# Optimization experiments

Hardware: AMD Instinct MI355X
Metric: run time of the kernel (lower is better)

## Reference

```python
import jax, jax.numpy as jnp
import numpy as np

B, S, D, H = 2, 2048, 1024, 16
DK = D // H


def setup_inputs() -> dict:
    key = jax.random.key(0)
    ks = jax.random.split(key, 7)
    q = jax.random.normal(ks[0], (B, S, D), dtype=jnp.float32)
    k = jax.random.normal(ks[1], (B, S, D), dtype=jnp.float32)
    v = jax.random.normal(ks[2], (B, S, D), dtype=jnp.float32)
    # causal mask, broadcastable [B,1,S,S]; masked_fill where mask==0
    mask = jnp.broadcast_to(jnp.tril(jnp.ones((S, S), dtype=jnp.int32)), (B, 1, S, S))
    scale = 0.02
    Wq = jax.random.normal(ks[3], (D, D), dtype=jnp.float32) * scale
    Wk = jax.random.normal(ks[4], (D, D), dtype=jnp.float32) * scale
    Wv = jax.random.normal(ks[5], (D, D), dtype=jnp.float32) * scale
    Wo = jax.random.normal(ks[6], (D, D), dtype=jnp.float32) * scale
    return {"q": q, "k": k, "v": v, "mask": mask, "Wq": Wq, "Wk": Wk, "Wv": Wv, "Wo": Wo}


def reference(q, k, v, mask, Wq, Wk, Wv, Wo):
    # torch nn.Linear(bias=False): y = x @ W.T with W of shape [out, in]
    def proj(x, W):
        return (x @ W.T).reshape(B, S, H, DK).transpose(0, 2, 1, 3)  # [B,H,S,DK]

    Q = proj(q, Wq)
    K = proj(k, Wk)
    V = proj(v, Wv)
    inv_sqrt_dk = np.float32(1.0 / np.sqrt(DK))
    scores = jnp.einsum('bhqd,bhkd->bhqk', Q, K) * inv_sqrt_dk  # [B,H,S,S]
    scores = jnp.where(mask == 0, jnp.float32(-jnp.inf), scores)
    attn = jax.nn.softmax(scores, axis=-1)
    x = jnp.einsum('bhqk,bhkd->bhqd', attn, V)  # [B,H,S,DK]
    x = x.transpose(0, 2, 1, 3).reshape(B, S, D)
    return x @ Wo.T
```

## Files before the change

kernel.cpp:

```cpp
#include <hip/hip_runtime.h>

typedef __bf16 bf16x8 __attribute__((ext_vector_type(8)));
typedef __bf16 bf16x2 __attribute__((ext_vector_type(2)));
typedef float  f32x4  __attribute__((ext_vector_type(4)));

#define DEV static __device__ __forceinline__
#define VMCNT(n) asm volatile("s_waitcnt vmcnt(" #n ")" ::: "memory")
#define LGKM0()  asm volatile("s_waitcnt lgkmcnt(0)" ::: "memory")
#define SBAR()   __builtin_amdgcn_s_barrier()
#define SFENCE() __builtin_amdgcn_sched_barrier(0)


DEV ushort f2bf(float f) {
    return __builtin_bit_cast(ushort, (__bf16)f);
}
DEV uint pk2(float a, float b) {
    bf16x2 t; t[0] = (__bf16)a; t[1] = (__bf16)b;
    return __builtin_bit_cast(uint, t);
}

DEV float redmax4(float x) {
    x = fmaxf(x, __shfl_xor(x, 16));
    return fmaxf(x, __shfl_xor(x, 32));
}
DEV float redsum4(float x) {
    x += __shfl_xor(x, 16);
    return x + __shfl_xor(x, 32);
}

DEV void stage_swz(const ushort* g, int gstride, char* lds, int nchunks) {
    const int tid  = threadIdx.x;
    const int lane = tid & 63;
    const int wave = tid >> 6;
    for (int c0 = wave * 64; c0 < nchunks; c0 += 256) {
        int c   = c0 + lane;
        int row = c >> 3;
        int cc  = (c & 7) ^ (row & 7);
        const ushort* src = g + row * gstride + cc * 8;
        __builtin_amdgcn_global_load_lds((__attribute__((address_space(1))) void*)src,
                                         (__attribute__((address_space(3))) void*)(lds + c0 * 16),
                                         16, 0, 0);
    }
}

DEV bf16x8 ldfrag(const char* tile, int row, int kc) {
    int off = (row << 7) + ((kc ^ (row & 7)) << 4);
    return *(const bf16x8*)(tile + off);
}


struct CvtArgs { const float* s[7]; ushort* d[7]; int n[7]; };

__global__ void cvt_kernel(CvtArgs a) {
    const int y = blockIdx.y;
    const float* __restrict__ s = a.s[y];
    ushort* __restrict__ d = a.d[y];
    const int n = a.n[y];
    const int stride = gridDim.x * blockDim.x;
    for (int i = blockIdx.x * blockDim.x + threadIdx.x; i * 8 < n; i += stride) {
        const float4* p = (const float4*)(s + (size_t)i * 8);
        float4 x = p[0], yv = p[1];
        uint4 o;
        o.x = pk2(x.x,  x.y);
        o.y = pk2(x.z,  x.w);
        o.z = pk2(yv.x, yv.y);
        o.w = pk2(yv.z, yv.w);
        *(uint4*)(d + (size_t)i * 8) = o;
    }
}


constexpr int GN = 1024, GK = 1024;

template<typename EPI>
DEV void gemm_body(const ushort* __restrict__ A, const ushort* __restrict__ W,
                   char* smem, EPI epi) {
    const int tid  = threadIdx.x;
    const int lane = tid & 63;
    const int w    = tid >> 6;
    const int wr   = w >> 1, wc = w & 1;
    const int hi   = lane >> 4, lj = lane & 15;
    const int nb   = blockIdx.x & 7, mb = blockIdx.x >> 3;

    f32x4 acc[4][4];
#pragma unroll
    for (int mi = 0; mi < 4; mi++)
#pragma unroll
        for (int ni = 0; ni < 4; ni++) acc[mi][ni] = f32x4{0.f, 0.f, 0.f, 0.f};

    const ushort* Ag = A + (size_t)mb * 128 * GK;
    const ushort* Wg = W + (size_t)nb * 128 * GK;

    for (int k0 = 0; k0 < GK; k0 += 64) {
        __syncthreads();
        stage_swz(Ag + k0, GK, smem, 1024);
        stage_swz(Wg + k0, GK, smem + 16384, 1024);
        __syncthreads();
#pragma unroll
        for (int kk = 0; kk < 2; ++kk) {
            bf16x8 a[4], b[4];
#pragma unroll
            for (int mi = 0; mi < 4; mi++) a[mi] = ldfrag(smem, wr * 64 + mi * 16 + lj, kk * 4 + hi);
#pragma unroll
            for (int ni = 0; ni < 4; ni++) b[ni] = ldfrag(smem + 16384, wc * 64 + ni * 16 + lj, kk * 4 + hi);
#pragma unroll
            for (int mi = 0; mi < 4; mi++)
#pragma unroll
                for (int ni = 0; ni < 4; ni++)
                    acc[mi][ni] = __builtin_amdgcn_mfma_f32_16x16x32_bf16(a[mi], b[ni], acc[mi][ni], 0, 0, 0);
        }
    }

#pragma unroll
    for (int mi = 0; mi < 4; mi++)
#pragma unroll
        for (int r = 0; r < 4; r++) {
            const int gm = mb * 128 + wr * 64 + mi * 16 + hi * 4 + r;
#pragma unroll
            for (int ni = 0; ni < 4; ni++) {
                const int gn = nb * 128 + wc * 64 + ni * 16 + lj;
                epi(gm, gn, acc[mi][ni][r]);
            }
        }
}

struct ProjArgs {
    const ushort* A[3]; const ushort* W[3]; ushort* O[3];
    float scale[3]; int mode[3];
};

__global__ __launch_bounds__(256, 3) void gemm_proj(ProjArgs args) {
    __shared__ char smem[32768];
    const int z = blockIdx.z;
    const ushort* A = args.A[z];
    const ushort* W = args.W[z];
    ushort* Out = args.O[z];
    const float scale = args.scale[z];
    const int mode = args.mode[z];
    gemm_body(A, W, smem, [&](int gm, int gn, float v) {
        v *= scale;
        const int b_ = gm >> 11, s_ = gm & 2047;
        const int h_ = gn >> 6,  d_ = gn & 63;
        size_t off;
        if (mode == 0) off = (((size_t)b_ * 16 + h_) * 2048 + s_) * 64 + d_;
        else           off = (((size_t)b_ * 16 + h_) * 64 + d_) * 2048 + s_;
        Out[off] = f2bf(v);
    });
}

__global__ __launch_bounds__(256, 3) void gemm_out(const ushort* __restrict__ A,
                                                   const ushort* __restrict__ W,
                                                   float* __restrict__ Out) {
    __shared__ char smem[32768];
    gemm_body(A, W, smem, [&](int gm, int gn, float v) {
        Out[(size_t)gm * GN + gn] = v;
    });
}


__global__ __launch_bounds__(256, 3) void attn_kernel(const ushort* __restrict__ Qb,
                                                      const ushort* __restrict__ Kb,
                                                      const ushort* __restrict__ Vt,
                                                      ushort* __restrict__ Xb,
                                                      float* __restrict__ Opart,
                                                      float* __restrict__ Mlp) {
    constexpr int S = 2048;
    __shared__ char smem[49152];
    const int tid = threadIdx.x, lane = tid & 63, w = tid >> 6;
    const int hi = lane >> 4, lj = lane & 15;
    char* Pw = smem + 32768 + w * 4096;
    const int bh = blockIdx.x;
    const int y = blockIdx.y;

    int qt, kts, kte, half;
    bool partial;
    if (y < 16) {
        qt = 15 - (y >> 1); half = y & 1; partial = true;
        if (half == 0) { kts = 0; kte = qt + 1; }
        else           { kts = qt + 1; kte = 2 * qt + 2; }
    } else {
        qt = 23 - y; half = 0; partial = false;
        kts = 0; kte = 2 * qt + 2;
    }
    const int q0 = qt * 128;
    const int q0w = q0 + w * 32;

    const ushort* Qg = Qb + (size_t)bh * S * 64;
    const ushort* Kg = Kb + (size_t)bh * S * 64;
    const ushort* Vg = Vt + (size_t)bh * 64 * S;

    bf16x8 qf[2][2];
#pragma unroll
    for (int mi = 0; mi < 2; mi++)
#pragma unroll
        for (int kk = 0; kk < 2; kk++)
            qf[mi][kk] = *(const bf16x8*)(Qg + (size_t)(q0w + mi * 16 + lj) * 64 + kk * 32 + hi * 8);

    f32x4 o[2][4];
    float m_run[2] = { -1e30f, -1e30f }, l_run[2] = { 0.f, 0.f };
#pragma unroll
    for (int mi = 0; mi < 2; mi++)
#pragma unroll
        for (int nd = 0; nd < 4; nd++) o[mi][nd] = f32x4{0.f, 0.f, 0.f, 0.f};

    stage_swz(Kg + (size_t)kts * 64 * 64, 64, smem, 512);
    stage_swz(Vg + kts * 64, S, smem + 16384, 512);
    int cur = 0;

    for (int t = kts; t < kte; ++t) {
        char* Kc = smem + (cur << 13);
        char* Vc = smem + 16384 + (cur << 13);
        if (t + 1 < kte) {
            stage_swz(Kg + (size_t)(t + 1) * 64 * 64, 64, smem + ((cur ^ 1) << 13), 512);
            stage_swz(Vg + (t + 1) * 64, S, smem + 16384 + ((cur ^ 1) << 13), 512);
            VMCNT(4);
        } else {
            VMCNT(0);
        }
        SBAR(); SFENCE();

        if (t * 64 <= q0w + 31) {
            f32x4 sc[2][4];
#pragma unroll
            for (int mi = 0; mi < 2; mi++)
#pragma unroll
                for (int ni = 0; ni < 4; ni++) sc[mi][ni] = f32x4{0.f, 0.f, 0.f, 0.f};
            __builtin_amdgcn_s_setprio(1);
#pragma unroll
            for (int kk = 0; kk < 2; ++kk) {
                bf16x8 kf[4];
#pragma unroll
                for (int ni = 0; ni < 4; ni++) kf[ni] = ldfrag(Kc, ni * 16 + lj, kk * 4 + hi);
#pragma unroll
                for (int mi = 0; mi < 2; mi++)
#pragma unroll
                    for (int ni = 0; ni < 4; ni++)
                        sc[mi][ni] = __builtin_amdgcn_mfma_f32_16x16x32_bf16(kf[ni], qf[mi][kk], sc[mi][ni], 0, 0, 0);
            }
            __builtin_amdgcn_s_setprio(0);

            const bool diag = (t * 64 + 63 > q0w);
#pragma unroll
            for (int mi = 0; mi < 2; mi++) {
                const int q = q0w + mi * 16 + lj;
                if (diag) {
#pragma unroll
                    for (int ni = 0; ni < 4; ni++)
#pragma unroll
                        for (int r = 0; r < 4; r++)
                            if (t * 64 + ni * 16 + hi * 4 + r > q) sc[mi][ni][r] = -1e30f;
                }
                float mx = -1e30f;
#pragma unroll
                for (int ni = 0; ni < 4; ni++)
#pragma unroll
                    for (int r = 0; r < 4; r++) mx = fmaxf(mx, sc[mi][ni][r]);
                mx = redmax4(mx);
                const float mo = m_run[mi];
                const bool defer = __all(mx <= mo + 8.f);
                float mn, rs;
                if (defer) { mn = mo; rs = 1.f; }
                else { mn = fmaxf(mo, mx); rs = __builtin_exp2f(mo - mn); m_run[mi] = mn; }
                float ps = 0.f;
                const int row = mi * 16 + lj;
#pragma unroll
                for (int ni = 0; ni < 4; ni++) {
                    float p0 = __builtin_exp2f(sc[mi][ni][0] - mn);
                    float p1 = __builtin_exp2f(sc[mi][ni][1] - mn);
                    float p2 = __builtin_exp2f(sc[mi][ni][2] - mn);
                    float p3 = __builtin_exp2f(sc[mi][ni][3] - mn);
                    ps += (p0 + p1) + (p2 + p3);
                    uint2 pv; pv.x = pk2(p0, p1); pv.y = pk2(p2, p3);
                    const int c = ni * 2 + (hi >> 1);
                    *(uint2*)(Pw + row * 128 + ((c ^ (row & 7)) << 4) + ((hi & 1) << 3)) = pv;
                }
                ps = redsum4(ps);
                if (defer) {
                    l_run[mi] += ps;
                } else {
                    l_run[mi] = l_run[mi] * rs + ps;
#pragma unroll
                    for (int r = 0; r < 4; r++) {
                        float rr = __shfl(rs, (lane & 48) | (hi * 4 + r));
#pragma unroll
                        for (int nd = 0; nd < 4; nd++) o[mi][nd][r] *= rr;
                    }
                }
            }

            LGKM0(); SFENCE();

            __builtin_amdgcn_s_setprio(1);
#pragma unroll
            for (int kk = 0; kk < 2; ++kk) {
                bf16x8 pa[2], bv[4];
#pragma unroll
                for (int mi = 0; mi < 2; mi++) pa[mi] = ldfrag(Pw, mi * 16 + lj, kk * 4 + hi);
#pragma unroll
                for (int nd = 0; nd < 4; nd++) bv[nd] = ldfrag(Vc, nd * 16 + lj, kk * 4 + hi);
#pragma unroll
                for (int mi = 0; mi < 2; mi++)
#pragma unroll
                    for (int nd = 0; nd < 4; nd++)
                        o[mi][nd] = __builtin_amdgcn_mfma_f32_16x16x32_bf16(pa[mi], bv[nd], o[mi][nd], 0, 0, 0);
            }
            __builtin_amdgcn_s_setprio(0);
        }

        LGKM0();
        SBAR(); SFENCE();
        cur ^= 1;
    }

    if (partial) {
        const int pidx = (((bh << 3) + (qt - 8)) << 1) + half;
        float* Op = Opart + (size_t)pidx * 8192;
        float* Ml = Mlp   + (size_t)pidx * 256;
#pragma unroll
        for (int mi = 0; mi < 2; mi++)
#pragma unroll
            for (int r = 0; r < 4; r++) {
                const int row = w * 32 + mi * 16 + hi * 4 + r;
#pragma unroll
                for (int nd = 0; nd < 4; nd++)
                    Op[row * 64 + nd * 16 + lj] = o[mi][nd][r];
            }
        if (hi == 0) {
#pragma unroll
            for (int mi = 0; mi < 2; mi++) {
                const int row = w * 32 + mi * 16 + lj;
                Ml[row * 2 + 0] = m_run[mi];
                Ml[row * 2 + 1] = l_run[mi];
            }
        }
    } else {
        const int b_ = bh >> 4, h_ = bh & 15;
#pragma unroll
        for (int mi = 0; mi < 2; mi++)
#pragma unroll
            for (int r = 0; r < 4; r++) {
                float lv = __shfl(l_run[mi], (lane & 48) | (hi * 4 + r));
                float inv = 1.f / lv;
                const int srow = q0w + mi * 16 + hi * 4 + r;
#pragma unroll
                for (int nd = 0; nd < 4; nd++)
                    Xb[((size_t)b_ * S + srow) * 1024 + h_ * 64 + nd * 16 + lj] =
                        f2bf(o[mi][nd][r] * inv);
            }
    }
}


__global__ __launch_bounds__(256) void attn_merge(const float* __restrict__ Op,
                                                  const float* __restrict__ Ml,
                                                  ushort* __restrict__ Xb) {
    const int bh = blockIdx.x;
    const int qt = 8 + blockIdx.y;
    const int tid = threadIdx.x;
    const int row = tid >> 1;
    const int c0 = (tid & 1) * 32;
    const int sbase = (((bh << 3) + (qt - 8)) << 1);
    const float* o0 = Op + (size_t)(sbase + 0) * 8192 + row * 64 + c0;
    const float* o1 = Op + (size_t)(sbase + 1) * 8192 + row * 64 + c0;
    const float* ml0 = Ml + (size_t)(sbase + 0) * 256 + row * 2;
    const float* ml1 = Ml + (size_t)(sbase + 1) * 256 + row * 2;
    const float m0 = ml0[0], l0 = ml0[1];
    const float m1 = ml1[0], l1 = ml1[1];
    const float m = fmaxf(m0, m1);
    const float a0 = __builtin_exp2f(m0 - m), a1 = __builtin_exp2f(m1 - m);
    const float inv = 1.f / (l0 * a0 + l1 * a1);
    const int b_ = bh >> 4, h_ = bh & 15;
    ushort* dst = Xb + ((size_t)b_ * 2048 + qt * 128 + row) * 1024 + h_ * 64 + c0;
#pragma unroll
    for (int c = 0; c < 32; c += 4) {
        float4 x = *(const float4*)(o0 + c);
        float4 y = *(const float4*)(o1 + c);
        uint2 pv;
        pv.x = pk2((x.x * a0 + y.x * a1) * inv, (x.y * a0 + y.y * a1) * inv);
        pv.y = pk2((x.z * a0 + y.z * a1) * inv, (x.w * a0 + y.w * a1) * inv);
        *(uint2*)(dst + c) = pv;
    }
}


extern "C" void kernel_launch(void* const* d_in, const int* in_sizes, int n_in,
                              void* d_out, int out_size, void* d_ws, size_t ws_size,
                              hipStream_t stream) {
    (void)in_sizes; (void)n_in; (void)out_size; (void)ws_size;
    const float* q  = (const float*)d_in[0];
    const float* k  = (const float*)d_in[1];
    const float* v  = (const float*)d_in[2];
    const float* Wq = (const float*)d_in[4];
    const float* Wk = (const float*)d_in[5];
    const float* Wv = (const float*)d_in[6];
    const float* Wo = (const float*)d_in[7];

    char* ws = (char*)d_ws;
    const size_t MB = (size_t)1 << 20;
    ushort* Qb  = (ushort*)(ws + 0 * MB);
    ushort* Kb  = (ushort*)(ws + 8 * MB);
    ushort* Vtb = (ushort*)(ws + 16 * MB);
    ushort* Xb  = (ushort*)(ws + 24 * MB);
    ushort* qb  = (ushort*)(ws + 32 * MB);
    ushort* kb  = (ushort*)(ws + 40 * MB);
    ushort* vb  = (ushort*)(ws + 48 * MB);
    ushort* Wqb = (ushort*)(ws + 56 * MB);
    ushort* Wkb = (ushort*)(ws + 58 * MB);
    ushort* Wvb = (ushort*)(ws + 60 * MB);
    ushort* Wob = (ushort*)(ws + 62 * MB);
    float*  Opart = (float*)(ws + 32 * MB);
    float*  Mlp   = (float*)(ws + 48 * MB);

    CvtArgs c;
    c.s[0] = q;  c.s[1] = k;  c.s[2] = v;  c.s[3] = Wq;  c.s[4] = Wk;  c.s[5] = Wv;  c.s[6] = Wo;
    c.d[0] = qb; c.d[1] = kb; c.d[2] = vb; c.d[3] = Wqb; c.d[4] = Wkb; c.d[5] = Wvb; c.d[6] = Wob;
    c.n[0] = c.n[1] = c.n[2] = 4 * 1024 * 1024;
    c.n[3] = c.n[4] = c.n[5] = c.n[6] = 1024 * 1024;
    cvt_kernel<<<dim3(1024, 7), 256, 0, stream>>>(c);

    ProjArgs p;
    p.A[0] = qb;  p.A[1] = kb;  p.A[2] = vb;
    p.W[0] = Wqb; p.W[1] = Wkb; p.W[2] = Wvb;
    p.O[0] = Qb;  p.O[1] = Kb;  p.O[2] = Vtb;
    p.scale[0] = 0.125f * 1.44269504088896f;
    p.scale[1] = 1.0f; p.scale[2] = 1.0f;
    p.mode[0] = 0; p.mode[1] = 0; p.mode[2] = 1;
    gemm_proj<<<dim3(256, 1, 3), 256, 0, stream>>>(p);

    attn_kernel<<<dim3(32, 24), 256, 0, stream>>>(Qb, Kb, Vtb, Xb, Opart, Mlp);
    attn_merge<<<dim3(32, 8), 256, 0, stream>>>(Opart, Mlp, Xb);

    gemm_out<<<256, 256, 0, stream>>>(Xb, Wob, (float*)d_out);
}
```

Baseline: 255.9 us.

## Fuse fp32 activation conversion into projection GEMM and rebalance attention splits

The projection GEMM now stages fp32 activations straight into LDS and converts to bf16 while loading fragments, so the separate activation conversion pass and its bf16 round trip through memory go away. Only the weights are still converted beforehand. Attention work is split into up to four KV slices per query tile depending on causal length, giving 40 y-blocks instead of 24 for better load balance. Partial outputs are stored in bf16 and the merge kernel combines a variable number of slices. GEMM block order is also swizzled. The trade-offs are doubled LDS use in the projection, which may lower occupancy, extra conversion ALU work in the inner loop, and some precision loss in the partials.

```diff
diff --git a/kernel.cpp b/kernel.cpp
--- a/kernel.cpp
+++ b/kernel.cpp
@@ -43,21 +43,44 @@
     }
 }
 
+DEV void stage_swz32(const float* g, int gstride, char* lds, int nchunks) {
+    const int tid  = threadIdx.x;
+    const int lane = tid & 63;
+    const int wave = tid >> 6;
+    for (int c0 = wave * 64; c0 < nchunks; c0 += 256) {
+        int c   = c0 + lane;
+        int row = c >> 4;
+        int cc  = (c & 15) ^ (row & 15);
+        const float* src = g + row * gstride + cc * 4;
+        __builtin_amdgcn_global_load_lds((__attribute__((address_space(1))) void*)src,
+                                         (__attribute__((address_space(3))) void*)(lds + c0 * 16),
+                                         16, 0, 0);
+    }
+}
+
 DEV bf16x8 ldfrag(const char* tile, int row, int kc) {
     int off = (row << 7) + ((kc ^ (row & 7)) << 4);
     return *(const bf16x8*)(tile + off);
 }
 
-
-struct CvtArgs { const float* s[7]; ushort* d[7]; int n[7]; };
+DEV bf16x8 ldfrag32(const char* tile, int row, int cl0) {
+    const int base = row << 8, rs = row & 15;
+    f32x4 v0 = *(const f32x4*)(tile + base + ((cl0 ^ rs) << 4));
+    f32x4 v1 = *(const f32x4*)(tile + base + (((cl0 + 1) ^ rs) << 4));
+    uint4 u;
+    u.x = pk2(v0[0], v0[1]); u.y = pk2(v0[2], v0[3]);
+    u.z = pk2(v1[0], v1[1]); u.w = pk2(v1[2], v1[3]);
+    return __builtin_bit_cast(bf16x8, u);
+}
+
+
+struct CvtArgs { const float* s[4]; ushort* d[4]; int n; };
 
 __global__ void cvt_kernel(CvtArgs a) {
-    const int y = blockIdx.y;
-    const float* __restrict__ s = a.s[y];
-    ushort* __restrict__ d = a.d[y];
-    const int n = a.n[y];
+    const float* __restrict__ s = a.s[blockIdx.y];
+    ushort* __restrict__ d = a.d[blockIdx.y];
     const int stride = gridDim.x * blockDim.x;
-    for (int i = blockIdx.x * blockDim.x + threadIdx.x; i * 8 < n; i += stride) {
+    for (int i = blockIdx.x * blockDim.x + threadIdx.x; i * 8 < a.n; i += stride) {
         const float4* p = (const float4*)(s + (size_t)i * 8);
         float4 x = p[0], yv = p[1];
         uint4 o;
@@ -69,18 +92,93 @@
     }
 }
 
-
 constexpr int GN = 1024, GK = 1024;
 
-template<typename EPI>
-DEV void gemm_body(const ushort* __restrict__ A, const ushort* __restrict__ W,
-                   char* smem, EPI epi) {
+
+struct ProjArgs {
+    const float* A[3]; const ushort* W[3]; ushort* O[3];
+    float scale[3]; int mode[3];
+};
+
+__global__ __launch_bounds__(256, 3) void gemm_proj(ProjArgs args) {
+    __shared__ char smem[49152];
+    const int z = blockIdx.z;
+    const float* A = args.A[z];
+    const ushort* W = args.W[z];
+    ushort* Out = args.O[z];
+    const float scale = args.scale[z];
+    const int mode = args.mode[z];
+
     const int tid  = threadIdx.x;
     const int lane = tid & 63;
     const int w    = tid >> 6;
     const int wr   = w >> 1, wc = w & 1;
     const int hi   = lane >> 4, lj = lane & 15;
-    const int nb   = blockIdx.x & 7, mb = blockIdx.x >> 3;
+    const int g    = blockIdx.x;
+    const int o_   = ((g & 7) << 5) | (g >> 3);
+    const int nb   = o_ & 7, mb = o_ >> 3;
+
+    f32x4 acc[4][4];
+#pragma unroll
+    for (int mi = 0; mi < 4; mi++)
+#pragma unroll
+        for (int ni = 0; ni < 4; ni++) acc[mi][ni] = f32x4{0.f, 0.f, 0.f, 0.f};
+
+    const float*  Ag = A + (size_t)mb * 128 * GK;
+    const ushort* Wg = W + (size_t)nb * 128 * GK;
+
+    for (int k0 = 0; k0 < GK; k0 += 64) {
+        __syncthreads();
+        stage_swz32(Ag + k0, GK, smem, 2048);
+        stage_swz(Wg + k0, GK, smem + 32768, 1024);
+        __syncthreads();
+#pragma unroll
+        for (int kk = 0; kk < 2; ++kk) {
+            bf16x8 a[4], b[4];
+#pragma unroll
+            for (int mi = 0; mi < 4; mi++) a[mi] = ldfrag32(smem, wr * 64 + mi * 16 + lj, kk * 8 + hi * 2);
+#pragma unroll
+            for (int ni = 0; ni < 4; ni++) b[ni] = ldfrag(smem + 32768, wc * 64 + ni * 16 + lj, kk * 4 + hi);
+#pragma unroll
+            for (int mi = 0; mi < 4; mi++)
+#pragma unroll
+                for (int ni = 0; ni < 4; ni++)
+                    acc[mi][ni] = __builtin_amdgcn_mfma_f32_16x16x32_bf16(a[mi], b[ni], acc[mi][ni], 0, 0, 0);
+        }
+    }
+
+#pragma unroll
+    for (int mi = 0; mi < 4; mi++)
+#pragma unroll
+        for (int r = 0; r < 4; r++) {
+            const int gm = mb * 128 + wr * 64 + mi * 16 + hi * 4 + r;
+            const int b_ = gm >> 11, s_ = gm & 2047;
+#pragma unroll
+            for (int ni = 0; ni < 4; ni++) {
+                const int gn = nb * 128 + wc * 64 + ni * 16 + lj;
+                const int h_ = gn >> 6, d_ = gn & 63;
+                float v = acc[mi][ni][r] * scale;
+                size_t off;
+                if (mode == 0) off = (((size_t)b_ * 16 + h_) * 2048 + s_) * 64 + d_;
+                else           off = (((size_t)b_ * 16 + h_) * 64 + d_) * 2048 + s_;
+                Out[off] = f2bf(v);
+            }
+        }
+}
+
+
+__global__ __launch_bounds__(256, 3) void gemm_out(const ushort* __restrict__ A,
+                                                   const ushort* __restrict__ W,
+                                                   float* __restrict__ Out) {
+    __shared__ char smem[32768];
+    const int tid  = threadIdx.x;
+    const int lane = tid & 63;
+    const int w    = tid >> 6;
+    const int wr   = w >> 1, wc = w & 1;
+    const int hi   = lane >> 4, lj = lane & 15;
+    const int g    = blockIdx.x;
+    const int o_   = ((g & 7) << 5) | (g >> 3);
+    const int nb   = o_ & 7, mb = o_ >> 3;
 
     f32x4 acc[4][4];
 #pragma unroll
@@ -119,42 +217,9 @@
 #pragma unroll
             for (int ni = 0; ni < 4; ni++) {
                 const int gn = nb * 128 + wc * 64 + ni * 16 + lj;
-                epi(gm, gn, acc[mi][ni][r]);
-            }
-        }
-}
-
-struct ProjArgs {
-    const ushort* A[3]; const ushort* W[3]; ushort* O[3];
-    float scale[3]; int mode[3];
-};
-
-__global__ __launch_bounds__(256, 3) void gemm_proj(ProjArgs args) {
-    __shared__ char smem[32768];
-    const int z = blockIdx.z;
-    const ushort* A = args.A[z];
-    const ushort* W = args.W[z];
-    ushort* Out = args.O[z];
-    const float scale = args.scale[z];
-    const int mode = args.mode[z];
-    gemm_body(A, W, smem, [&](int gm, int gn, float v) {
-        v *= scale;
-        const int b_ = gm >> 11, s_ = gm & 2047;
-        const int h_ = gn >> 6,  d_ = gn & 63;
-        size_t off;
-        if (mode == 0) off = (((size_t)b_ * 16 + h_) * 2048 + s_) * 64 + d_;
-        else           off = (((size_t)b_ * 16 + h_) * 64 + d_) * 2048 + s_;
-        Out[off] = f2bf(v);
-    });
-}
-
-__global__ __launch_bounds__(256, 3) void gemm_out(const ushort* __restrict__ A,
-                                                   const ushort* __restrict__ W,
-                                                   float* __restrict__ Out) {
-    __shared__ char smem[32768];
-    gemm_body(A, W, smem, [&](int gm, int gn, float v) {
-        Out[(size_t)gm * GN + gn] = v;
-    });
+                Out[(size_t)gm * GN + gn] = acc[mi][ni][r];
+            }
+        }
 }
 
 
@@ -162,7 +227,7 @@
                                                       const ushort* __restrict__ Kb,
                                                       const ushort* __restrict__ Vt,
                                                       ushort* __restrict__ Xb,
-                                                      float* __restrict__ Opart,
+                                                      ushort* __restrict__ Opart,
                                                       float* __restrict__ Mlp) {
     constexpr int S = 2048;
     __shared__ char smem[49152];
@@ -172,16 +237,16 @@
     const int bh = blockIdx.x;
     const int y = blockIdx.y;
 
-    int qt, kts, kte, half;
-    bool partial;
-    if (y < 16) {
-        qt = 15 - (y >> 1); half = y & 1; partial = true;
-        if (half == 0) { kts = 0; kte = qt + 1; }
-        else           { kts = qt + 1; kte = 2 * qt + 2; }
-    } else {
-        qt = 23 - y; half = 0; partial = false;
-        kts = 0; kte = 2 * qt + 2;
-    }
+    int qt, slice, nsl;
+    if (y < 16)      { qt = 12 + (y & 3);            slice = y >> 2;        nsl = 4; }
+    else if (y < 28) { int zz = y - 16; qt = 8 + (zz & 3); slice = zz >> 2; nsl = 3; }
+    else if (y < 36) { int zz = y - 28; qt = 4 + (zz & 3); slice = zz >> 2; nsl = 2; }
+    else             { qt = y - 36;                  slice = 0;             nsl = 1; }
+    const int nt  = 2 * qt + 2;
+    const int kts = (nt * slice) / nsl;
+    const int kte = (nt * (slice + 1)) / nsl;
+    const bool partial = (nsl > 1);
+
     const int q0 = qt * 128;
     const int q0w = q0 + w * 32;
 
@@ -313,9 +378,9 @@
     }
 
     if (partial) {
-        const int pidx = (((bh << 3) + (qt - 8)) << 1) + half;
-        float* Op = Opart + (size_t)pidx * 8192;
-        float* Ml = Mlp   + (size_t)pidx * 256;
+        const int pidx = bh * 40 + y;
+        ushort* Op = Opart + (size_t)pidx * 8192;
+        float*  Ml = Mlp   + (size_t)pidx * 256;
 #pragma unroll
         for (int mi = 0; mi < 2; mi++)
 #pragma unroll
@@ -323,7 +388,7 @@
                 const int row = w * 32 + mi * 16 + hi * 4 + r;
 #pragma unroll
                 for (int nd = 0; nd < 4; nd++)
-                    Op[row * 64 + nd * 16 + lj] = o[mi][nd][r];
+                    Op[row * 64 + nd * 16 + lj] = f2bf(o[mi][nd][r]);
             }
         if (hi == 0) {
 #pragma unroll
@@ -351,35 +416,46 @@
 }
 
 
-__global__ __launch_bounds__(256) void attn_merge(const float* __restrict__ Op,
+__global__ __launch_bounds__(256) void attn_merge(const ushort* __restrict__ Op,
                                                   const float* __restrict__ Ml,
                                                   ushort* __restrict__ Xb) {
     const int bh = blockIdx.x;
-    const int qt = 8 + blockIdx.y;
+    const int qt = 4 + blockIdx.y;
+    const int nsl  = (qt < 8) ? 2 : (qt < 12) ? 3 : 4;
+    const int ybase = (qt >= 12) ? (qt - 12) : (qt >= 8) ? (16 + qt - 8) : (28 + qt - 4);
     const int tid = threadIdx.x;
     const int row = tid >> 1;
     const int c0 = (tid & 1) * 32;
-    const int sbase = (((bh << 3) + (qt - 8)) << 1);
-    const float* o0 = Op + (size_t)(sbase + 0) * 8192 + row * 64 + c0;
-    const float* o1 = Op + (size_t)(sbase + 1) * 8192 + row * 64 + c0;
-    const float* ml0 = Ml + (size_t)(sbase + 0) * 256 + row * 2;
-    const float* ml1 = Ml + (size_t)(sbase + 1) * 256 + row * 2;
-    const float m0 = ml0[0], l0 = ml0[1];
-    const float m1 = ml1[0], l1 = ml1[1];
-    const float m = fmaxf(m0, m1);
-    const float a0 = __builtin_exp2f(m0 - m), a1 = __builtin_exp2f(m1 - m);
-    const float inv = 1.f / (l0 * a0 + l1 * a1);
+
+    float ms[4], ls[4];
+    float m = -1e30f;
+    for (int s = 0; s < nsl; ++s) {
+        const int slot = bh * 40 + ybase + s * 4;
+        ms[s] = Ml[(size_t)slot * 256 + row * 2 + 0];
+        ls[s] = Ml[(size_t)slot * 256 + row * 2 + 1];
+        m = fmaxf(m, ms[s]);
+    }
+    float acc[32];
+#pragma unroll
+    for (int c = 0; c < 32; ++c) acc[c] = 0.f;
+    float l = 0.f;
+    for (int s = 0; s < nsl; ++s) {
+        const float a = __builtin_exp2f(ms[s] - m);
+        l += ls[s] * a;
+        const ushort* op = Op + (size_t)(bh * 40 + ybase + s * 4) * 8192 + row * 64 + c0;
+#pragma unroll
+        for (int c8 = 0; c8 < 32; c8 += 8) {
+            bf16x8 v = *(const bf16x8*)(op + c8);
+#pragma unroll
+            for (int e = 0; e < 8; ++e) acc[c8 + e] += a * (float)v[e];
+        }
+    }
+    const float inv = 1.f / l;
     const int b_ = bh >> 4, h_ = bh & 15;
     ushort* dst = Xb + ((size_t)b_ * 2048 + qt * 128 + row) * 1024 + h_ * 64 + c0;
 #pragma unroll
-    for (int c = 0; c < 32; c += 4) {
-        float4 x = *(const float4*)(o0 + c);
-        float4 y = *(const float4*)(o1 + c);
-        uint2 pv;
-        pv.x = pk2((x.x * a0 + y.x * a1) * inv, (x.y * a0 + y.y * a1) * inv);
-        pv.y = pk2((x.z * a0 + y.z * a1) * inv, (x.w * a0 + y.w * a1) * inv);
-        *(uint2*)(dst + c) = pv;
-    }
+    for (int c = 0; c < 32; c += 2)
+        *(uint*)(dst + c) = pk2(acc[c] * inv, acc[c + 1] * inv);
 }
 
 
@@ -397,29 +473,25 @@
 
     char* ws = (char*)d_ws;
     const size_t MB = (size_t)1 << 20;
-    ushort* Qb  = (ushort*)(ws + 0 * MB);
-    ushort* Kb  = (ushort*)(ws + 8 * MB);
-    ushort* Vtb = (ushort*)(ws + 16 * MB);
-    ushort* Xb  = (ushort*)(ws + 24 * MB);
-    ushort* qb  = (ushort*)(ws + 32 * MB);
-    ushort* kb  = (ushort*)(ws + 40 * MB);
-    ushort* vb  = (ushort*)(ws + 48 * MB);
-    ushort* Wqb = (ushort*)(ws + 56 * MB);
-    ushort* Wkb = (ushort*)(ws + 58 * MB);
-    ushort* Wvb = (ushort*)(ws + 60 * MB);
-    ushort* Wob = (ushort*)(ws + 62 * MB);
-    float*  Opart = (float*)(ws + 32 * MB);
-    float*  Mlp   = (float*)(ws + 48 * MB);
+    ushort* Qb   = (ushort*)(ws + 0 * MB);
+    ushort* Kb   = (ushort*)(ws + 8 * MB);
+    ushort* Vtb  = (ushort*)(ws + 16 * MB);
+    ushort* Xb   = (ushort*)(ws + 24 * MB);
+    ushort* Wqb  = (ushort*)(ws + 32 * MB);
+    ushort* Wkb  = (ushort*)(ws + 34 * MB);
+    ushort* Wvb  = (ushort*)(ws + 36 * MB);
+    ushort* Wob  = (ushort*)(ws + 38 * MB);
+    ushort* Opart= (ushort*)(ws + 40 * MB);
+    float*  Mlp  = (float*) (ws + 60 * MB);
 
     CvtArgs c;
-    c.s[0] = q;  c.s[1] = k;  c.s[2] = v;  c.s[3] = Wq;  c.s[4] = Wk;  c.s[5] = Wv;  c.s[6] = Wo;
-    c.d[0] = qb; c.d[1] = kb; c.d[2] = vb; c.d[3] = Wqb; c.d[4] = Wkb; c.d[5] = Wvb; c.d[6] = Wob;
-    c.n[0] = c.n[1] = c.n[2] = 4 * 1024 * 1024;
-    c.n[3] = c.n[4] = c.n[5] = c.n[6] = 1024 * 1024;
-    cvt_kernel<<<dim3(1024, 7), 256, 0, stream>>>(c);
+    c.s[0] = Wq;  c.s[1] = Wk;  c.s[2] = Wv;  c.s[3] = Wo;
+    c.d[0] = Wqb; c.d[1] = Wkb; c.d[2] = Wvb; c.d[3] = Wob;
+    c.n = 1024 * 1024;
+    cvt_kernel<<<dim3(512, 4), 256, 0, stream>>>(c);
 
     ProjArgs p;
-    p.A[0] = qb;  p.A[1] = kb;  p.A[2] = vb;
+    p.A[0] = q;   p.A[1] = k;   p.A[2] = v;
     p.W[0] = Wqb; p.W[1] = Wkb; p.W[2] = Wvb;
     p.O[0] = Qb;  p.O[1] = Kb;  p.O[2] = Vtb;
     p.scale[0] = 0.125f * 1.44269504088896f;
@@ -427,8 +499,8 @@
     p.mode[0] = 0; p.mode[1] = 0; p.mode[2] = 1;
     gemm_proj<<<dim3(256, 1, 3), 256, 0, stream>>>(p);
 
-    attn_kernel<<<dim3(32, 24), 256, 0, stream>>>(Qb, Kb, Vtb, Xb, Opart, Mlp);
-    attn_merge<<<dim3(32, 8), 256, 0, stream>>>(Opart, Mlp, Xb);
+    attn_kernel<<<dim3(32, 40), 256, 0, stream>>>(Qb, Kb, Vtb, Xb, Opart, Mlp);
+    attn_merge<<<dim3(32, 12), 256, 0, stream>>>(Opart, Mlp, Xb);
 
     gemm_out<<<256, 256, 0, stream>>>(Xb, Wob, (float*)d_out);
 }
```

Measured after the change: 248.3 us. 3.0% less time.
